# Performance work log

Measured on AMD Instinct MI355X. Metric: run time of the kernel, lower is better.

Reference implementation:

```python
import jax, jax.numpy as jnp
import numpy as np
import math

B, S, E, HEAD = 4, 2048, 1024, 64  # num_heads=16 -> head_size = 1024//16


def setup_inputs() -> dict:
    key = jax.random.key(0)
    kx, kp, kq, kk, kv = jax.random.split(key, 5)
    std = math.sqrt(2.0 / (E + HEAD))
    return {
        "x": jax.random.normal(kx, (B, S, E), dtype=jnp.float32),
        "padding_mask": jax.random.randint(kp, (B, S), 0, 2, dtype=jnp.int32),
        "Wq": jax.random.normal(kq, (HEAD, E), dtype=jnp.float32) * std,
        "Wk": jax.random.normal(kk, (HEAD, E), dtype=jnp.float32) * std,
        "Wv": jax.random.normal(kv, (HEAD, E), dtype=jnp.float32) * std,
    }


def reference(x, padding_mask, Wq, Wk, Wv):
    # q,k,v: [B,S,head] via Linear (x @ W.T, no bias)
    q = jnp.einsum("bse,he->bsh", x, Wq)
    k = jnp.einsum("bse,he->bsh", x, Wk)
    v = jnp.einsum("bse,he->bsh", x, Wv)
    scores = jnp.einsum("bqh,bkh->bqk", q, k)  # [B,S,S]
    seq = x.shape[1]
    causal = jnp.tril(jnp.ones((seq, seq), dtype=jnp.float32))  # [S,S]
    mask = causal[None, :, :] * padding_mask.astype(jnp.float32)[:, None, :]  # [B,S,S]
    scores = jnp.where(mask == 0, jnp.float32(-1e9), scores)
    head_size = k.shape[-1]
    attn = jax.nn.softmax(scores / jnp.sqrt(jnp.float32(head_size)), axis=-1)
    return jnp.einsum("bqk,bkh->bqh", attn, v)
```

## Files before the change

kernel.cpp:

```cpp
#include <hip/hip_runtime.h>
#include <hip/hip_bf16.h>
#include <math.h>

#define B_ 4
#define S_ 2048
#define E_ 1024
#define H_ 64
#define NQT 32
#define SPLITS 8
#define TPS 4

typedef short bf16x8 __attribute__((ext_vector_type(8)));
typedef float f32x4 __attribute__((ext_vector_type(4)));
typedef unsigned short u16x8 __attribute__((ext_vector_type(8)));
typedef unsigned short u16x4 __attribute__((ext_vector_type(4)));

__device__ __forceinline__ unsigned short f2bf(float f){
    unsigned u = __builtin_bit_cast(unsigned, f);
    u += 0x7fffu + ((u >> 16) & 1u);
    return (unsigned short)(u >> 16);
}
__device__ __forceinline__ float bf2f(unsigned short h){
    return __builtin_bit_cast(float, ((unsigned)h) << 16);
}
#define MFMA16(a,b,c) __builtin_amdgcn_mfma_f32_16x16x32_bf16((a),(b),(c),0,0,0)

__global__ __launch_bounds__(256) void qkv_kernel(
    const float* __restrict__ x, const float* __restrict__ Wq,
    const float* __restrict__ Wk, const float* __restrict__ Wv,
    unsigned short* __restrict__ Qhi, unsigned short* __restrict__ Qlo,
    unsigned short* __restrict__ Khi, unsigned short* __restrict__ Klo,
    unsigned short* __restrict__ Vt)
{
    __shared__ unsigned short Ah[64*64], Al[64*64], Bh[64*64], Bl[64*64];
    const int m0 = blockIdx.x * 64;
    const int comp = blockIdx.y;
    const float* W = (comp==0) ? Wq : (comp==1) ? Wk : Wv;
    const int tid = threadIdx.x;
    const int lane = tid & 63, wv = tid >> 6, l15 = lane & 15, quad = lane >> 4;

    f32x4 acc[4];
    #pragma unroll
    for (int i=0;i<4;i++) acc[i] = f32x4{0.f,0.f,0.f,0.f};

    const int arow = tid >> 2;
    const int ag0  = (tid & 3) * 2;

    for (int k0 = 0; k0 < E_; k0 += 64) {
        const float* xs = x + (size_t)(m0 + arow)*E_ + k0 + ag0*8;
        float4 xa = ((const float4*)xs)[0];
        float4 xb = ((const float4*)xs)[1];
        float4 xc = ((const float4*)xs)[2];
        float4 xd = ((const float4*)xs)[3];
        const float* wsrc = W + (size_t)arow*E_ + k0 + ag0*8;
        float4 wa = ((const float4*)wsrc)[0];
        float4 wb = ((const float4*)wsrc)[1];
        float4 wc = ((const float4*)wsrc)[2];
        float4 wd = ((const float4*)wsrc)[3];
        __syncthreads();
        auto put = [&](unsigned short* hi_t, unsigned short* lo_t, int g, float4 p, float4 q2){
            u16x8 hv, lv;
            float vv[8] = {p.x,p.y,p.z,p.w,q2.x,q2.y,q2.z,q2.w};
            #pragma unroll
            for (int j=0;j<8;j++){ unsigned short h = f2bf(vv[j]); hv[j]=h; lv[j]=f2bf(vv[j]-bf2f(h)); }
            int idx = arow*8 + (g ^ (arow & 7));
            ((u16x8*)hi_t)[idx] = hv; ((u16x8*)lo_t)[idx] = lv;
        };
        put(Ah, Al, ag0,   xa, xb);
        put(Ah, Al, ag0+1, xc, xd);
        put(Bh, Bl, ag0,   wa, wb);
        put(Bh, Bl, ag0+1, wc, wd);
        __syncthreads();
        #pragma unroll
        for (int kk=0; kk<2; kk++){
            const int arw = wv*16 + l15;
            bf16x8 ah = ((const bf16x8*)Ah)[arw*8 + ((kk*4+quad) ^ (l15 & 7))];
            bf16x8 al = ((const bf16x8*)Al)[arw*8 + ((kk*4+quad) ^ (l15 & 7))];
            #pragma unroll
            for (int nt=0; nt<4; nt++){
                const int brw = nt*16 + l15;
                bf16x8 bh = ((const bf16x8*)Bh)[brw*8 + ((kk*4+quad) ^ (l15 & 7))];
                bf16x8 bl = ((const bf16x8*)Bl)[brw*8 + ((kk*4+quad) ^ (l15 & 7))];
                acc[nt] = MFMA16(ah, bh, acc[nt]);
                acc[nt] = MFMA16(ah, bl, acc[nt]);
                acc[nt] = MFMA16(al, bh, acc[nt]);
            }
        }
    }
    if (comp < 2) {
        unsigned short* dh = (comp==0) ? Qhi : Khi;
        unsigned short* dl = (comp==0) ? Qlo : Klo;
        #pragma unroll
        for (int nt=0; nt<4; nt++)
        #pragma unroll
        for (int r=0; r<4; r++){
            int row = m0 + wv*16 + quad*4 + r;
            float v = acc[nt][r];
            unsigned short h = f2bf(v);
            dh[(size_t)row*H_ + nt*16 + l15] = h;
            dl[(size_t)row*H_ + nt*16 + l15] = f2bf(v - bf2f(h));
        }
    } else {
        int b = m0 >> 11;
        int s0 = (m0 & (S_-1)) + wv*16 + quad*4;
        #pragma unroll
        for (int nt=0; nt<4; nt++){
            u16x4 pk;
            #pragma unroll
            for (int r=0;r<4;r++) pk[r] = f2bf(acc[nt][r]);
            *(u16x4*)(Vt + (size_t)b*H_*S_ + (size_t)(nt*16+l15)*S_ + s0) = pk;
        }
    }
}

__global__ __launch_bounds__(256) void meanv_kernel(const unsigned short* __restrict__ Vt,
                                                    float* __restrict__ meanV)
{
    int b = blockIdx.x >> 6, h = blockIdx.x & 63;
    const unsigned short* src = Vt + (size_t)b*H_*S_ + (size_t)h*S_;
    float sum = 0.f;
    for (int j = threadIdx.x; j < S_; j += 256) sum += bf2f(src[j]);
    #pragma unroll
    for (int m=32; m>=1; m>>=1) sum += __shfl_xor(sum, m);
    __shared__ float red[4];
    if ((threadIdx.x & 63) == 0) red[threadIdx.x >> 6] = sum;
    __syncthreads();
    if (threadIdx.x == 0) meanV[b*H_ + h] = (red[0]+red[1]+red[2]+red[3]) * (1.f/S_);
}

__global__ __launch_bounds__(256) void attn_kernel(
    const unsigned short* __restrict__ Qhi, const unsigned short* __restrict__ Qlo,
    const unsigned short* __restrict__ Khi, const unsigned short* __restrict__ Klo,
    const unsigned short* __restrict__ Vt, const int* __restrict__ pad,
    float* __restrict__ Opart, float* __restrict__ mpart, float* __restrict__ lpart)
{
    const int qt = blockIdx.x, b = blockIdx.y, sp = blockIdx.z;
    const int t0 = sp * TPS;
    if (t0 > qt) return;
    const int t1 = min(t0 + TPS, qt + 1);

    __shared__ unsigned short KtH[64*64], KtL[64*64], Vts[64*64];
    __shared__ unsigned short Ps[4][64*20];
    __shared__ int pad_s[64];

    const int tid = threadIdx.x, lane = tid & 63, wv = tid >> 6, l15 = lane & 15, quad = lane >> 4;
    const int role = tid >> 6, srow = tid & 63;

    const size_t qrow = (size_t)(b*S_ + qt*64 + wv*16 + l15);
    bf16x8 aqh0 = *(const bf16x8*)(Qhi + qrow*H_ + quad*8);
    bf16x8 aqh1 = *(const bf16x8*)(Qhi + qrow*H_ + 32 + quad*8);
    bf16x8 aql0 = *(const bf16x8*)(Qlo + qrow*H_ + quad*8);
    bf16x8 aql1 = *(const bf16x8*)(Qlo + qrow*H_ + 32 + quad*8);

    float m_i[4], l_i[4];
    f32x4 o[4];
    #pragma unroll
    for (int r=0;r<4;r++){ m_i[r] = -INFINITY; l_i[r] = 0.f; }
    #pragma unroll
    for (int i=0;i<4;i++) o[i] = f32x4{0.f,0.f,0.f,0.f};

    const int qg = qt*64 + wv*16 + quad*4;
    unsigned short* Pw = &Ps[wv][0];

    for (int t = t0; t < t1; ++t) {
        const int kb = t * 64;
        __syncthreads();
        if (role < 3) {
            const unsigned short* gs =
                (role==0) ? (Khi + ((size_t)(b*S_ + kb + srow))*H_) :
                (role==1) ? (Klo + ((size_t)(b*S_ + kb + srow))*H_) :
                            (Vt + (size_t)b*H_*S_ + (size_t)srow*S_ + kb);
            unsigned short* ld = (role==0) ? KtH : (role==1) ? KtL : Vts;
            #pragma unroll
            for (int i=0;i<8;i++){
                u16x8 d = ((const u16x8*)gs)[i];
                ((u16x8*)ld)[srow*8 + (i ^ (srow & 7))] = d;
            }
        } else {
            pad_s[srow] = pad[b*S_ + kb + srow];
        }
        __syncthreads();

        f32x4 s[4];
        #pragma unroll
        for (int nt=0; nt<4; nt++){
            const int krw = nt*16 + l15;
            bf16x8 bh0 = ((const bf16x8*)KtH)[krw*8 + ((quad)   ^ (l15 & 7))];
            bf16x8 bh1 = ((const bf16x8*)KtH)[krw*8 + ((4+quad) ^ (l15 & 7))];
            bf16x8 bl0 = ((const bf16x8*)KtL)[krw*8 + ((quad)   ^ (l15 & 7))];
            bf16x8 bl1 = ((const bf16x8*)KtL)[krw*8 + ((4+quad) ^ (l15 & 7))];
            f32x4 z = f32x4{0.f,0.f,0.f,0.f};
            z = MFMA16(aqh0, bh0, z);
            z = MFMA16(aqh1, bh1, z);
            z = MFMA16(aqh0, bl0, z);
            z = MFMA16(aqh1, bl1, z);
            z = MFMA16(aql0, bh0, z);
            z = MFMA16(aql1, bh1, z);
            s[nt] = z;
        }
        float rmax[4] = {-INFINITY,-INFINITY,-INFINITY,-INFINITY};
        #pragma unroll
        for (int nt=0; nt<4; nt++){
            const int kcol = nt*16 + l15;
            const int kg = kb + kcol;
            const int pv = pad_s[kcol];
            #pragma unroll
            for (int r=0;r<4;r++){
                bool ok = (kg <= qg + r) && (pv != 0);
                float v = ok ? s[nt][r]*0.125f : -1.25e8f;
                s[nt][r] = v;
                rmax[r] = fmaxf(rmax[r], v);
            }
        }
        #pragma unroll
        for (int msk=1; msk<=8; msk<<=1){
            #pragma unroll
            for (int r=0;r<4;r++) rmax[r] = fmaxf(rmax[r], __shfl_xor(rmax[r], msk));
        }
        float alpha[4];
        #pragma unroll
        for (int r=0;r<4;r++){
            float mn = fmaxf(m_i[r], rmax[r]);
            alpha[r] = __expf(m_i[r] - mn);
            m_i[r] = mn;
        }
        float rsum[4] = {0.f,0.f,0.f,0.f};
        #pragma unroll
        for (int nt=0; nt<4; nt++)
        #pragma unroll
        for (int r=0;r<4;r++){
            float p = __expf(s[nt][r] - m_i[r]);
            s[nt][r] = p;
            rsum[r] += p;
        }
        #pragma unroll
        for (int msk=1; msk<=8; msk<<=1){
            #pragma unroll
            for (int r=0;r<4;r++) rsum[r] += __shfl_xor(rsum[r], msk);
        }
        #pragma unroll
        for (int r=0;r<4;r++) l_i[r] = l_i[r]*alpha[r] + rsum[r];
        #pragma unroll
        for (int hnt=0; hnt<4; hnt++)
        #pragma unroll
        for (int r=0;r<4;r++) o[hnt][r] *= alpha[r];

        #pragma unroll
        for (int nt=0; nt<4; nt++){
            const int key = nt*16 + l15;
            u16x4 pk;
            #pragma unroll
            for (int r=0;r<4;r++) pk[r] = f2bf(s[nt][r]);
            *(u16x4*)(Pw + key*20 + quad*4) = pk;
        }
        #pragma unroll
        for (int ks=0; ks<2; ks++){
            bf16x8 ap;
            #pragma unroll
            for (int j=0;j<8;j++) ap[j] = (short)Pw[(ks*32 + quad*8 + j)*20 + l15];
            #pragma unroll
            for (int hnt=0; hnt<4; hnt++){
                bf16x8 bv = ((const bf16x8*)Vts)[(hnt*16+l15)*8 + ((ks*4+quad) ^ (l15 & 7))];
                o[hnt] = MFMA16(ap, bv, o[hnt]);
            }
        }
    }
    const size_t rbase = ((size_t)((b*NQT + qt)*SPLITS + sp))*64 + wv*16 + quad*4;
    if (l15 == 0) {
        #pragma unroll
        for (int r=0;r<4;r++){ mpart[rbase + r] = m_i[r]; lpart[rbase + r] = l_i[r]; }
    }
    #pragma unroll
    for (int hnt=0; hnt<4; hnt++)
    #pragma unroll
    for (int r=0;r<4;r++)
        Opart[(rbase + r)*H_ + hnt*16 + l15] = o[hnt][r];
}

__global__ __launch_bounds__(256) void combine_kernel(
    const float* __restrict__ Opart, const float* __restrict__ mpart,
    const float* __restrict__ lpart, const float* __restrict__ meanV,
    float* __restrict__ out)
{
    const int idx = blockIdx.x*256 + threadIdx.x;
    const int h = idx & 63;
    const int q = (idx >> 6) & (S_-1);
    const int b = idx >> 17;
    const int qt = q >> 6, r = q & 63;
    const int ns = (qt >> 2) + 1;
    const size_t rb = ((size_t)(b*NQT + qt)*SPLITS)*64 + r;
    float M = -INFINITY;
    for (int s2=0; s2<ns; s2++) M = fmaxf(M, mpart[rb + (size_t)s2*64]);
    float res;
    if (M == -1.25e8f) {
        res = meanV[b*H_ + h];
    } else {
        float L = 0.f, acc = 0.f;
        for (int s2=0; s2<ns; s2++){
            float mi = mpart[rb + (size_t)s2*64];
            float wgt = __expf(mi - M);
            L += wgt * lpart[rb + (size_t)s2*64];
            acc += wgt * Opart[(rb + (size_t)s2*64)*H_ + h];
        }
        res = acc / L;
    }
    out[idx] = res;
}

extern "C" void kernel_launch(void* const* d_in, const int* in_sizes, int n_in,
                              void* d_out, int out_size, void* d_ws, size_t ws_size,
                              hipStream_t stream)
{
    (void)in_sizes; (void)n_in; (void)out_size; (void)ws_size;
    const float* x  = (const float*)d_in[0];
    const int* pad  = (const int*)d_in[1];
    const float* Wq = (const float*)d_in[2];
    const float* Wk = (const float*)d_in[3];
    const float* Wv = (const float*)d_in[4];
    float* out = (float*)d_out;
    char* ws = (char*)d_ws;
    const size_t MB = 1u << 20;
    unsigned short* Qhi = (unsigned short*)(ws + 0*MB);
    unsigned short* Qlo = (unsigned short*)(ws + 1*MB);
    unsigned short* Khi = (unsigned short*)(ws + 2*MB);
    unsigned short* Klo = (unsigned short*)(ws + 3*MB);
    unsigned short* Vt  = (unsigned short*)(ws + 4*MB);
    float* Opart = (float*)(ws + 5*MB);
    float* mpart = (float*)(ws + 21*MB);
    float* lpart = (float*)(ws + 21*MB + (1u<<18));
    float* meanV = (float*)(ws + 21*MB + 2*(1u<<18));

    qkv_kernel<<<dim3(128,3), 256, 0, stream>>>(x, Wq, Wk, Wv, Qhi, Qlo, Khi, Klo, Vt);
    meanv_kernel<<<dim3(256), 256, 0, stream>>>(Vt, meanV);
    attn_kernel<<<dim3(NQT, B_, SPLITS), 256, 0, stream>>>(Qhi, Qlo, Khi, Klo, Vt, pad,
                                                           Opart, mpart, lpart);
    combine_kernel<<<dim3((B_*S_*H_)/256), 256, 0, stream>>>(Opart, mpart, lpart, meanV, out);
}
```

Measured before the change: 137.0 us.

## Fuse Q/K/V projections per block with pre-split bf16 weights loaded via LDS DMA

Adds a weight-prep kernel that splits Wq/Wk/Wv into pre-swizzled bf16 hi/lo arrays once per call. The QKV kernel now takes 32 rows of x per block and computes all three projections together (192 output columns, each wave owning 48 of them). The x tile is converted to hi/lo once and shared across Q, K and V instead of being reloaded and reconverted three times. Weights are streamed straight into LDS with global_load_lds, avoiding per-iteration float-to-bf16 conversion of W. The cost is an extra kernel launch and more LDS per block (B tile of 192 rows).

```diff
diff --git a/kernel.cpp b/kernel.cpp
--- a/kernel.cpp
+++ b/kernel.cpp
@@ -25,90 +25,130 @@
 }
 #define MFMA16(a,b,c) __builtin_amdgcn_mfma_f32_16x16x32_bf16((a),(b),(c),0,0,0)
 
+__device__ __forceinline__ void gload_lds16(const void* g, void* l){
+    __builtin_amdgcn_global_load_lds((const __attribute__((address_space(1))) unsigned int*)g,
+                                     (__attribute__((address_space(3))) unsigned int*)l, 16, 0, 0);
+}
+
+__global__ __launch_bounds__(256) void wprep_kernel(
+    const float* __restrict__ Wq, const float* __restrict__ Wk,
+    const float* __restrict__ Wv,
+    unsigned short* __restrict__ WhiS, unsigned short* __restrict__ WloS)
+{
+    const int gid = blockIdx.x*256 + threadIdx.x;
+    const int n = gid >> 7, g = gid & 127;
+    const float* W = (n < 64)  ? (Wq + (size_t)n*E_)
+                   : (n < 128) ? (Wk + (size_t)(n-64)*E_)
+                               : (Wv + (size_t)(n-128)*E_);
+    const int gs = (g & ~7) | ((g & 7) ^ (n & 7));
+    const float* src = W + gs*8;
+    float4 a = ((const float4*)src)[0];
+    float4 b = ((const float4*)src)[1];
+    float vv[8] = {a.x,a.y,a.z,a.w,b.x,b.y,b.z,b.w};
+    u16x8 hv, lv;
+    #pragma unroll
+    for (int j=0;j<8;j++){ unsigned short h = f2bf(vv[j]); hv[j]=h; lv[j]=f2bf(vv[j]-bf2f(h)); }
+    ((u16x8*)WhiS)[n*128 + g] = hv;
+    ((u16x8*)WloS)[n*128 + g] = lv;
+}
+
 __global__ __launch_bounds__(256) void qkv_kernel(
-    const float* __restrict__ x, const float* __restrict__ Wq,
-    const float* __restrict__ Wk, const float* __restrict__ Wv,
+    const float* __restrict__ x,
+    const unsigned short* __restrict__ WhiS, const unsigned short* __restrict__ WloS,
     unsigned short* __restrict__ Qhi, unsigned short* __restrict__ Qlo,
     unsigned short* __restrict__ Khi, unsigned short* __restrict__ Klo,
     unsigned short* __restrict__ Vt)
 {
-    __shared__ unsigned short Ah[64*64], Al[64*64], Bh[64*64], Bl[64*64];
-    const int m0 = blockIdx.x * 64;
-    const int comp = blockIdx.y;
-    const float* W = (comp==0) ? Wq : (comp==1) ? Wk : Wv;
+    __shared__ unsigned short Ah[32*64], Al[32*64];
+    __shared__ unsigned short Bh[192*64], Bl[192*64];
+    const int m0 = blockIdx.x * 32;
     const int tid = threadIdx.x;
     const int lane = tid & 63, wv = tid >> 6, l15 = lane & 15, quad = lane >> 4;
 
-    f32x4 acc[4];
-    #pragma unroll
-    for (int i=0;i<4;i++) acc[i] = f32x4{0.f,0.f,0.f,0.f};
-
-    const int arow = tid >> 2;
-    const int ag0  = (tid & 3) * 2;
+    f32x4 acc[2][3];
+    #pragma unroll
+    for (int mt=0;mt<2;mt++)
+    #pragma unroll
+    for (int nt=0;nt<3;nt++) acc[mt][nt] = f32x4{0.f,0.f,0.f,0.f};
+
+    const int arow = tid >> 3;
+    const int ag   = tid & 7;
+    unsigned short* tbuf = (wv < 2) ? Bh : Bl;
+    const unsigned short* gsrc = (wv < 2) ? WhiS : WloS;
+    const int rbase0 = (wv & 1) * 96;
+    const int lrow = lane >> 3, lgrp = lane & 7;
 
     for (int k0 = 0; k0 < E_; k0 += 64) {
-        const float* xs = x + (size_t)(m0 + arow)*E_ + k0 + ag0*8;
+        const float* xs = x + (size_t)(m0 + arow)*E_ + k0 + ag*8;
         float4 xa = ((const float4*)xs)[0];
         float4 xb = ((const float4*)xs)[1];
-        float4 xc = ((const float4*)xs)[2];
-        float4 xd = ((const float4*)xs)[3];
-        const float* wsrc = W + (size_t)arow*E_ + k0 + ag0*8;
-        float4 wa = ((const float4*)wsrc)[0];
-        float4 wb = ((const float4*)wsrc)[1];
-        float4 wc = ((const float4*)wsrc)[2];
-        float4 wd = ((const float4*)wsrc)[3];
         __syncthreads();
-        auto put = [&](unsigned short* hi_t, unsigned short* lo_t, int g, float4 p, float4 q2){
+        #pragma unroll
+        for (int i = 0; i < 12; i++) {
+            const int rb = rbase0 + i*8;
+            const unsigned short* gp = gsrc + (size_t)(rb + lrow)*E_ + k0 + lgrp*8;
+            gload_lds16(gp, tbuf + rb*64);
+        }
+        {
+            float vv[8] = {xa.x,xa.y,xa.z,xa.w,xb.x,xb.y,xb.z,xb.w};
             u16x8 hv, lv;
-            float vv[8] = {p.x,p.y,p.z,p.w,q2.x,q2.y,q2.z,q2.w};
             #pragma unroll
             for (int j=0;j<8;j++){ unsigned short h = f2bf(vv[j]); hv[j]=h; lv[j]=f2bf(vv[j]-bf2f(h)); }
-            int idx = arow*8 + (g ^ (arow & 7));
-            ((u16x8*)hi_t)[idx] = hv; ((u16x8*)lo_t)[idx] = lv;
-        };
-        put(Ah, Al, ag0,   xa, xb);
-        put(Ah, Al, ag0+1, xc, xd);
-        put(Bh, Bl, ag0,   wa, wb);
-        put(Bh, Bl, ag0+1, wc, wd);
+            const int idx = arow*8 + (ag ^ (arow & 7));
+            ((u16x8*)Ah)[idx] = hv; ((u16x8*)Al)[idx] = lv;
+        }
         __syncthreads();
         #pragma unroll
         for (int kk=0; kk<2; kk++){
-            const int arw = wv*16 + l15;
-            bf16x8 ah = ((const bf16x8*)Ah)[arw*8 + ((kk*4+quad) ^ (l15 & 7))];
-            bf16x8 al = ((const bf16x8*)Al)[arw*8 + ((kk*4+quad) ^ (l15 & 7))];
-            #pragma unroll
-            for (int nt=0; nt<4; nt++){
-                const int brw = nt*16 + l15;
-                bf16x8 bh = ((const bf16x8*)Bh)[brw*8 + ((kk*4+quad) ^ (l15 & 7))];
-                bf16x8 bl = ((const bf16x8*)Bl)[brw*8 + ((kk*4+quad) ^ (l15 & 7))];
-                acc[nt] = MFMA16(ah, bh, acc[nt]);
-                acc[nt] = MFMA16(ah, bl, acc[nt]);
-                acc[nt] = MFMA16(al, bh, acc[nt]);
-            }
-        }
-    }
-    if (comp < 2) {
-        unsigned short* dh = (comp==0) ? Qhi : Khi;
-        unsigned short* dl = (comp==0) ? Qlo : Klo;
-        #pragma unroll
-        for (int nt=0; nt<4; nt++)
-        #pragma unroll
-        for (int r=0; r<4; r++){
-            int row = m0 + wv*16 + quad*4 + r;
-            float v = acc[nt][r];
-            unsigned short h = f2bf(v);
-            dh[(size_t)row*H_ + nt*16 + l15] = h;
-            dl[(size_t)row*H_ + nt*16 + l15] = f2bf(v - bf2f(h));
-        }
-    } else {
-        int b = m0 >> 11;
-        int s0 = (m0 & (S_-1)) + wv*16 + quad*4;
-        #pragma unroll
-        for (int nt=0; nt<4; nt++){
-            u16x4 pk;
-            #pragma unroll
-            for (int r=0;r<4;r++) pk[r] = f2bf(acc[nt][r]);
-            *(u16x4*)(Vt + (size_t)b*H_*S_ + (size_t)(nt*16+l15)*S_ + s0) = pk;
+            const int xr = (kk*4+quad) ^ (l15 & 7);
+            bf16x8 ah[2], al[2];
+            #pragma unroll
+            for (int mt=0; mt<2; mt++){
+                const int arw = mt*16 + l15;
+                ah[mt] = ((const bf16x8*)Ah)[arw*8 + xr];
+                al[mt] = ((const bf16x8*)Al)[arw*8 + xr];
+            }
+            #pragma unroll
+            for (int nt=0; nt<3; nt++){
+                const int brw = wv*48 + nt*16 + l15;
+                bf16x8 bh = ((const bf16x8*)Bh)[brw*8 + xr];
+                bf16x8 bl = ((const bf16x8*)Bl)[brw*8 + xr];
+                #pragma unroll
+                for (int mt=0; mt<2; mt++){
+                    acc[mt][nt] = MFMA16(ah[mt], bh, acc[mt][nt]);
+                    acc[mt][nt] = MFMA16(ah[mt], bl, acc[mt][nt]);
+                    acc[mt][nt] = MFMA16(al[mt], bh, acc[mt][nt]);
+                }
+            }
+        }
+    }
+    #pragma unroll
+    for (int nt=0; nt<3; nt++){
+        const int n = wv*48 + nt*16 + l15;
+        const int comp = n >> 6, c = n & 63;
+        if (comp < 2) {
+            unsigned short* dh = (comp==0) ? Qhi : Khi;
+            unsigned short* dl = (comp==0) ? Qlo : Klo;
+            #pragma unroll
+            for (int mt=0; mt<2; mt++)
+            #pragma unroll
+            for (int r=0; r<4; r++){
+                const int row = m0 + mt*16 + quad*4 + r;
+                float v = acc[mt][nt][r];
+                unsigned short h = f2bf(v);
+                dh[(size_t)row*H_ + c] = h;
+                dl[(size_t)row*H_ + c] = f2bf(v - bf2f(h));
+            }
+        } else {
+            #pragma unroll
+            for (int mt=0; mt<2; mt++){
+                const int m = m0 + mt*16 + quad*4;
+                const int b = m >> 11, s0 = m & (S_-1);
+                u16x4 pk;
+                #pragma unroll
+                for (int r=0;r<4;r++) pk[r] = f2bf(acc[mt][nt][r]);
+                *(u16x4*)(Vt + (size_t)(b*H_ + c)*S_ + s0) = pk;
+            }
         }
     }
 }
@@ -329,8 +369,11 @@
     float* mpart = (float*)(ws + 21*MB);
     float* lpart = (float*)(ws + 21*MB + (1u<<18));
     float* meanV = (float*)(ws + 21*MB + 2*(1u<<18));
-
-    qkv_kernel<<<dim3(128,3), 256, 0, stream>>>(x, Wq, Wk, Wv, Qhi, Qlo, Khi, Klo, Vt);
+    unsigned short* WhiS = (unsigned short*)(ws + 22*MB);
+    unsigned short* WloS = (unsigned short*)(ws + 22*MB + 512*1024);
+
+    wprep_kernel<<<dim3(96), 256, 0, stream>>>(Wq, Wk, Wv, WhiS, WloS);
+    qkv_kernel<<<dim3(256), 256, 0, stream>>>(x, WhiS, WloS, Qhi, Qlo, Khi, Klo, Vt);
     meanv_kernel<<<dim3(256), 256, 0, stream>>>(Vt, meanV);
     attn_kernel<<<dim3(NQT, B_, SPLITS), 256, 0, stream>>>(Qhi, Qlo, Khi, Klo, Vt, pad,
                                                            Opart, mpart, lpart);
```

New measurement: 136.7 us, median of 2. No clear change (-0.3%).
